# Kernel tuning notes

Hardware: AMD Instinct MI355X
Metric: run time of the kernel (lower is better)

Reference implementation:

```python
import jax, jax.numpy as jnp
import numpy as np

D_MODEL = 1024
EXPAND = 2
D_INNER = EXPAND * D_MODEL  # 2048
D_STATE = 16
D_CONV = 4
DT_RANK = D_INNER  # non-int dt_rank resolves to d_inner
BATCH, SEQ = 2, 1024
EPS = 1e-5


def setup_inputs() -> dict:
    key = jax.random.key(0)
    ks = jax.random.split(key, 9)
    s = 0.02
    return {
        "x": jax.random.normal(ks[0], (BATCH, SEQ, D_MODEL), jnp.float32),
        "rms_w": jnp.ones((D_MODEL,), jnp.float32),
        "W_in": jax.random.normal(ks[1], (D_MODEL, 2 * D_INNER), jnp.float32) * s,
        "conv_w": jax.random.normal(ks[2], (D_INNER, 1, D_CONV), jnp.float32) * 0.2,
        "conv_b": jax.random.normal(ks[3], (D_INNER,), jnp.float32) * 0.02,
        "W_x": jax.random.normal(ks[4], (D_INNER, DT_RANK + 2 * D_STATE), jnp.float32) * s,
        "W_dt": jax.random.normal(ks[5], (DT_RANK, D_INNER), jnp.float32) * s,
        "A_log": jax.random.normal(ks[6], (D_INNER, D_STATE), jnp.float32),
        "W_out": jax.random.normal(ks[7], (D_INNER, D_MODEL), jnp.float32) * s,
    }


def _rmsnorm(x, w):
    var = jnp.mean(jnp.square(x), axis=-1, keepdims=True)
    return x * jax.lax.rsqrt(var + EPS) * w


def _forward(x, rms_w, W_in, conv_w, conv_b, W_x, W_dt, A_log, W_out):
    B, L, _ = x.shape
    residual = x
    xn = _rmsnorm(x, rms_w)
    xr = xn @ W_in                                  # [B,L,2*d_inner]
    xs, res = jnp.split(xr, 2, axis=-1)
    # causal depthwise conv1d: torch pads d_conv-1 both sides then slices [:L]
    xc = jnp.transpose(xs, (0, 2, 1))               # [B,d_inner,L]
    xc = jnp.pad(xc, ((0, 0), (0, 0), (D_CONV - 1, 0)))
    xc = jax.lax.conv_general_dilated(
        xc, conv_w, window_strides=(1,), padding='VALID',
        dimension_numbers=('NCH', 'OIH', 'NCH'), feature_group_count=D_INNER)
    xc = xc + conv_b[None, :, None]
    xs = jax.nn.silu(jnp.transpose(xc, (0, 2, 1)))  # [B,L,d_inner]
    x_ssm = xs @ W_x                                # [B,L,d_inner+2*d_state]
    dt, Bm, Cm = jnp.split(x_ssm, [D_INNER, D_INNER + D_STATE], axis=-1)
    dt = jax.nn.softplus(dt @ W_dt)                 # [B,L,d_inner]
    A = -jnp.exp(A_log)                             # [d_inner,d_state]
    A_disc = jnp.exp(A[None, None] * dt[..., None])            # [B,L,d_inner,N]
    Bx = dt[..., None] * Bm[:, :, None, :] * xs[..., None]     # [B,L,d_inner,N]

    def step(h, inp):
        Ad_t, Bx_t, C_t = inp                       # [B,d_inner,N],[B,d_inner,N],[B,N]
        h = Ad_t * h + Bx_t
        y = jnp.einsum('bdn,bn->bd', h, C_t)
        return h, y

    h0 = jnp.zeros((B, D_INNER, D_STATE), xs.dtype)
    _, ys = jax.lax.scan(
        step, h0,
        (jnp.transpose(A_disc, (1, 0, 2, 3)),
         jnp.transpose(Bx, (1, 0, 2, 3)),
         jnp.transpose(Cm, (1, 0, 2))))
    y = jnp.transpose(ys, (1, 0, 2))                # [B,L,d_inner]
    y = y * jax.nn.silu(res)
    out = y @ W_out
    return residual + out


def reference(x, rms_w, W_in, conv_w, conv_b, W_x, W_dt, A_log, W_out):
    return _forward(x, rms_w, W_in, conv_w, conv_b, W_x, W_dt, A_log, W_out)
```

## Files before the change

### kernel.cpp

```cpp
#include <hip/hip_runtime.h>
#include <math.h>

#define B_SZ   2
#define LSEQ   1024
#define DMODEL 1024
#define DINNER 2048
#define DSTATE 16
#define NTOK   (B_SZ * LSEQ)
#define NSSM   (DINNER + 2 * DSTATE)
#define CL     16
#define NCH    (LSEQ / CL)
#define NC     (B_SZ * DINNER)

typedef unsigned short ushort;
typedef __attribute__((ext_vector_type(8))) ushort ushort8;
typedef __attribute__((ext_vector_type(8))) __bf16 bf16x8;
typedef __attribute__((ext_vector_type(4))) float floatx4;

__device__ __forceinline__ float softplus_f(float x) {
  return (x > 20.f) ? x : __logf(1.f + __expf(x));
}
__device__ __forceinline__ float silu_f(float x) {
  return x / (1.f + __expf(-x));
}
__device__ __forceinline__ float bf2f(ushort u) {
  return __uint_as_float(((unsigned)u) << 16);
}
__device__ __forceinline__ ushort f2bf(float f) {
  unsigned u = __float_as_uint(f);
  return (ushort)((u + 0x7FFFu + ((u >> 16) & 1u)) >> 16);
}

__global__ __launch_bounds__(256) void rmsnorm_kernel(
    const float* __restrict__ x, const float* __restrict__ w,
    ushort* __restrict__ xn) {
  int row = blockIdx.x;
  const float* xrow = x + (size_t)row * DMODEL;
  float v[4];
  float ss = 0.f;
#pragma unroll
  for (int i = 0; i < 4; i++) {
    v[i] = xrow[threadIdx.x + 256 * i];
    ss += v[i] * v[i];
  }
  __shared__ float wsum[4];
  int lane = threadIdx.x & 63, wid = threadIdx.x >> 6;
#pragma unroll
  for (int off = 1; off < 64; off <<= 1) ss += __shfl_xor(ss, off);
  if (lane == 0) wsum[wid] = ss;
  __syncthreads();
  float tot = wsum[0] + wsum[1] + wsum[2] + wsum[3];
  float scale = rsqrtf(tot / (float)DMODEL + 1e-5f);
#pragma unroll
  for (int i = 0; i < 4; i++) {
    int j = threadIdx.x + 256 * i;
    xn[(size_t)row * DMODEL + j] = f2bf(v[i] * scale * w[j]);
  }
}

__global__ __launch_bounds__(256) void transpose_all(
    const float* __restrict__ Win, ushort* __restrict__ WinT,
    const float* __restrict__ Wx, ushort* __restrict__ WxT,
    const float* __restrict__ Wdt, ushort* __restrict__ WdtT,
    const float* __restrict__ Wout, ushort* __restrict__ WoutT) {
  int blk = blockIdx.x;
  const float* W; ushort* Wt; int K, N, nb, idx;
  if (blk < 1024)      { W = Win;  Wt = WinT;  K = DMODEL; N = 4096;  nb = 64; idx = blk; }
  else if (blk < 2080) { W = Wx;   Wt = WxT;   K = DINNER; N = NSSM;  nb = 33; idx = blk - 1024; }
  else if (blk < 3104) { W = Wdt;  Wt = WdtT;  K = DINNER; N = DINNER;nb = 32; idx = blk - 2080; }
  else                 { W = Wout; Wt = WoutT; K = DINNER; N = DMODEL;nb = 16; idx = blk - 3104; }
  int n0 = (idx % nb) * 64, k0 = (idx / nb) * 64;
  __shared__ float tile[64][65];
  int c = threadIdx.x & 63, rb = (threadIdx.x >> 6) << 4;
#pragma unroll
  for (int i = 0; i < 16; i++) {
    int k = k0 + rb + i;
    if (k < K && n0 + c < N) tile[rb + i][c] = W[(size_t)k * N + n0 + c];
  }
  __syncthreads();
#pragma unroll
  for (int i = 0; i < 16; i++) {
    int n = n0 + rb + i;
    if (n < N && k0 + c < K)
      Wt[(size_t)n * K + k0 + c] = f2bf(tile[c][rb + i]);
  }
}

__global__ __launch_bounds__(256, 3) void gemm_mfma(
    const ushort* __restrict__ A, int lda,
    const ushort* __restrict__ Bt, int ldb,
    int N, int K, int mode,
    void* __restrict__ C0, void* __restrict__ C1,
    const float* __restrict__ addend) {
  __shared__ ushort As[2 * 2 * 128 * 32];
  __shared__ ushort Bs[2 * 2 * 64 * 32];
  const int bm = blockIdx.y * 128, bn = blockIdx.x * 64;
  const int tid = threadIdx.x;
  const int wave = tid >> 6, lane = tid & 63;
  const int wm = (wave & 1) << 6, wn = (wave >> 1) << 5;
  const int lrow = lane & 15, quad = lane >> 4;
  const size_t koff = (size_t)blockIdx.z * K;

  const int sr = tid >> 2;
  const int q  = tid & 3;
  const int swr = (sr ^ (sr >> 2)) & 3;
  const int pq = (q ^ swr) << 3;
  const int brow = min(bn + sr, N - 1);
  const ushort* ga0 = A + (size_t)(bm + sr) * lda + koff + (q << 3);
  const ushort* ga1 = A + (size_t)(bm + sr + 64) * lda + koff + (q << 3);
  const ushort* gb0 = Bt + (size_t)brow * ldb + koff + (q << 3);

  floatx4 acc[4][2];
#pragma unroll
  for (int i = 0; i < 4; i++)
#pragma unroll
    for (int j = 0; j < 2; j++) acc[i][j] = (floatx4){0.f, 0.f, 0.f, 0.f};

  const int swf = ((lrow ^ (lrow >> 2)) & 3);
  const int fq = ((quad ^ swf) << 3);

  const int nk = K >> 6;
  ushort8 ra[2][2], rbv[2];
#pragma unroll
  for (int p = 0; p < 2; p++) {
    ra[p][0] = *(const ushort8*)(ga0 + p * 32);
    ra[p][1] = *(const ushort8*)(ga1 + p * 32);
    rbv[p]   = *(const ushort8*)(gb0 + p * 32);
  }
  for (int kt = 0; kt < nk; kt++) {
    const int boA = (kt & 1) << 13;
    const int boB = (kt & 1) << 12;
#pragma unroll
    for (int p = 0; p < 2; p++) {
      *(ushort8*)&As[boA + (p << 12) + sr * 32 + pq] = ra[p][0];
      *(ushort8*)&As[boA + (p << 12) + (sr + 64) * 32 + pq] = ra[p][1];
      *(ushort8*)&Bs[boB + (p << 11) + sr * 32 + pq] = rbv[p];
    }
    __syncthreads();
    if (kt + 1 < nk) {
      const int ko = (kt + 1) << 6;
#pragma unroll
      for (int p = 0; p < 2; p++) {
        ra[p][0] = *(const ushort8*)(ga0 + ko + p * 32);
        ra[p][1] = *(const ushort8*)(ga1 + ko + p * 32);
        rbv[p]   = *(const ushort8*)(gb0 + ko + p * 32);
      }
    }
#pragma unroll
    for (int p = 0; p < 2; p++) {
      bf16x8 af[4], bfr[2];
#pragma unroll
      for (int i = 0; i < 4; i++)
        af[i] = __builtin_bit_cast(bf16x8,
            *(const ushort8*)&As[boA + (p << 12) + (wm + i * 16 + lrow) * 32 + fq]);
#pragma unroll
      for (int j = 0; j < 2; j++)
        bfr[j] = __builtin_bit_cast(bf16x8,
            *(const ushort8*)&Bs[boB + (p << 11) + (wn + j * 16 + lrow) * 32 + fq]);
#pragma unroll
      for (int i = 0; i < 4; i++)
#pragma unroll
        for (int j = 0; j < 2; j++)
          acc[i][j] = __builtin_amdgcn_mfma_f32_16x16x32_bf16(
              af[i], bfr[j], acc[i][j], 0, 0, 0);
    }
  }
  const int m0 = bm + wm, n0 = bn + wn, rq = quad << 2;
  float* P = (float*)C0 + (size_t)blockIdx.z * NTOK * N;
#pragma unroll
  for (int i = 0; i < 4; i++) {
#pragma unroll
    for (int j = 0; j < 2; j++) {
#pragma unroll
      for (int r = 0; r < 4; r++) {
        int m = m0 + i * 16 + rq + r;
        int n = n0 + j * 16 + lrow;
        if (n >= N) continue;
        float v = acc[i][j][r];
        if (mode == 0) {
          P[(size_t)m * N + n] = v;
        } else if (mode == 1) {
          if (n < DINNER)
            ((ushort*)C0)[(size_t)m * DINNER + n] = f2bf(v);
          else
            ((ushort*)C1)[(size_t)m * DINNER + n - DINNER] = f2bf(silu_f(v));
        } else if (mode == 2) {
          ((ushort*)C0)[(size_t)m * NSSM + n] = f2bf(v);
          if (n >= DINNER)
            ((float*)C1)[(size_t)m * 32 + n - DINNER] = v;
        } else {
          ((float*)C0)[(size_t)m * DINNER + n] = softplus_f(v);
        }
      }
    }
  }
}

__global__ __launch_bounds__(256) void reduce_wout(
    const float* __restrict__ P, const float* __restrict__ x,
    float* __restrict__ out) {
  int gid = blockIdx.x * 256 + threadIdx.x;
  const float4 a = ((const float4*)P)[gid];
  const float4 b = ((const float4*)P)[gid + (NTOK * DMODEL / 4)];
  const float4 r = ((const float4*)x)[gid];
  ((float4*)out)[gid] = make_float4(a.x + b.x + r.x, a.y + b.y + r.y,
                                    a.z + b.z + r.z, a.w + b.w + r.w);
}

__global__ __launch_bounds__(256) void conv_silu_kernel(
    const ushort* __restrict__ xsraw, const float* __restrict__ cw,
    const float* __restrict__ cb, ushort* __restrict__ xs) {
  int gid = blockIdx.x * 256 + threadIdx.x;
  int c = gid & (DINNER - 1);
  int t = gid >> 11;
  int l = t & (LSEQ - 1);
  float w0 = cw[c * 4 + 0], w1 = cw[c * 4 + 1], w2 = cw[c * 4 + 2], w3 = cw[c * 4 + 3];
  const ushort* col = xsraw + (size_t)t * DINNER + c;
  float acc = cb[c] + w3 * bf2f(col[0]);
  if (l >= 1) acc += w2 * bf2f(col[-DINNER]);
  if (l >= 2) acc += w1 * bf2f(col[-2 * DINNER]);
  if (l >= 3) acc += w0 * bf2f(col[-3 * DINNER]);
  xs[gid] = f2bf(silu_f(acc));
}

__global__ __launch_bounds__(256) void scan_chunk1(
    const float* __restrict__ dt, const ushort* __restrict__ xs,
    const float* __restrict__ bc, const float* __restrict__ A_log,
    float* __restrict__ Bc, float* __restrict__ S) {
  int blk = blockIdx.x;
  int b = blk >> 9;
  int rem = blk & 511;
  int ch = rem >> 3;
  int dblk = rem & 7;
  int d = dblk * 256 + threadIdx.x;
  int c = b * DINNER + d;
  float a[DSTATE];
#pragma unroll
  for (int i = 0; i < 4; i++) {
    float4 v = *(const float4*)(A_log + (size_t)d * DSTATE + 4 * i);
    a[4 * i + 0] = -__expf(v.x);
    a[4 * i + 1] = -__expf(v.y);
    a[4 * i + 2] = -__expf(v.z);
    a[4 * i + 3] = -__expf(v.w);
  }
  float h[DSTATE] = {};
  float Ssum = 0.f;
  size_t t = (size_t)b * LSEQ + (size_t)ch * CL;
#pragma unroll 2
  for (int l = 0; l < CL; l++, t++) {
    float dtv = dt[t * DINNER + d];
    float dx = dtv * bf2f(xs[t * DINNER + d]);
    const float4* Bp = (const float4*)(bc + t * 32);
    float4 b0 = Bp[0], b1 = Bp[1], b2 = Bp[2], b3 = Bp[3];
    float bb[DSTATE] = {b0.x, b0.y, b0.z, b0.w, b1.x, b1.y, b1.z, b1.w,
                        b2.x, b2.y, b2.z, b2.w, b3.x, b3.y, b3.z, b3.w};
#pragma unroll
    for (int n = 0; n < DSTATE; n++)
      h[n] = __expf(a[n] * dtv) * h[n] + dx * bb[n];
    Ssum += dtv;
  }
  float4* outp = (float4*)(Bc + ((size_t)c * NCH + ch) * DSTATE);
  outp[0] = make_float4(h[0], h[1], h[2], h[3]);
  outp[1] = make_float4(h[4], h[5], h[6], h[7]);
  outp[2] = make_float4(h[8], h[9], h[10], h[11]);
  outp[3] = make_float4(h[12], h[13], h[14], h[15]);
  S[c * NCH + ch] = Ssum;
}

__global__ __launch_bounds__(256) void scan_combine(
    const float* __restrict__ A_log, const float* __restrict__ S,
    float* BcHin) {
  int gid = blockIdx.x * 256 + threadIdx.x;
  int c = gid >> 4, n = gid & 15;
  int d = c & (DINNER - 1);
  float a = -__expf(A_log[d * DSTATE + n]);
  float h = 0.f;
  size_t base = (size_t)c * (NCH * DSTATE) + n;
  for (int ch = 0; ch < NCH; ch++) {
    float bcv = BcHin[base + (size_t)ch * DSTATE];
    float decay = __expf(a * S[c * NCH + ch]);
    BcHin[base + (size_t)ch * DSTATE] = h;
    h = decay * h + bcv;
  }
}

__global__ __launch_bounds__(256) void scan_chunk2(
    const float* __restrict__ dt, const ushort* __restrict__ xs,
    const float* __restrict__ bc, const ushort* __restrict__ gate,
    const float* __restrict__ A_log, const float* __restrict__ hin,
    ushort* __restrict__ y) {
  int blk = blockIdx.x;
  int b = blk >> 9;
  int rem = blk & 511;
  int ch = rem >> 3;
  int dblk = rem & 7;
  int d = dblk * 256 + threadIdx.x;
  int c = b * DINNER + d;
  float a[DSTATE];
#pragma unroll
  for (int i = 0; i < 4; i++) {
    float4 v = *(const float4*)(A_log + (size_t)d * DSTATE + 4 * i);
    a[4 * i + 0] = -__expf(v.x);
    a[4 * i + 1] = -__expf(v.y);
    a[4 * i + 2] = -__expf(v.z);
    a[4 * i + 3] = -__expf(v.w);
  }
  float h[DSTATE];
  const float4* hi = (const float4*)(hin + ((size_t)c * NCH + ch) * DSTATE);
#pragma unroll
  for (int i = 0; i < 4; i++) {
    float4 v = hi[i];
    h[4 * i + 0] = v.x; h[4 * i + 1] = v.y; h[4 * i + 2] = v.z; h[4 * i + 3] = v.w;
  }
  size_t t = (size_t)b * LSEQ + (size_t)ch * CL;
#pragma unroll 2
  for (int l = 0; l < CL; l++, t++) {
    float dtv = dt[t * DINNER + d];
    float dx = dtv * bf2f(xs[t * DINNER + d]);
    const float4* Bp = (const float4*)(bc + t * 32);
    const float4* Cp = (const float4*)(bc + t * 32 + 16);
    float4 b0 = Bp[0], b1 = Bp[1], b2 = Bp[2], b3 = Bp[3];
    float4 c0 = Cp[0], c1 = Cp[1], c2 = Cp[2], c3 = Cp[3];
    float bb[DSTATE] = {b0.x, b0.y, b0.z, b0.w, b1.x, b1.y, b1.z, b1.w,
                        b2.x, b2.y, b2.z, b2.w, b3.x, b3.y, b3.z, b3.w};
    float cc[DSTATE] = {c0.x, c0.y, c0.z, c0.w, c1.x, c1.y, c1.z, c1.w,
                        c2.x, c2.y, c2.z, c2.w, c3.x, c3.y, c3.z, c3.w};
    float ysum = 0.f;
#pragma unroll
    for (int n = 0; n < DSTATE; n++) {
      h[n] = __expf(a[n] * dtv) * h[n] + dx * bb[n];
      ysum = fmaf(h[n], cc[n], ysum);
    }
    y[t * DINNER + d] = f2bf(ysum * bf2f(gate[t * DINNER + d]));
  }
}

extern "C" void kernel_launch(void* const* d_in, const int* in_sizes, int n_in,
                              void* d_out, int out_size, void* d_ws, size_t ws_size,
                              hipStream_t stream) {
  const float* x      = (const float*)d_in[0];
  const float* rms_w  = (const float*)d_in[1];
  const float* W_in   = (const float*)d_in[2];
  const float* conv_w = (const float*)d_in[3];
  const float* conv_b = (const float*)d_in[4];
  const float* W_x    = (const float*)d_in[5];
  const float* W_dt   = (const float*)d_in[6];
  const float* A_log  = (const float*)d_in[7];
  const float* W_out  = (const float*)d_in[8];
  float* out = (float*)d_out;

  char* w = (char*)d_ws;
  ushort* xnb   = (ushort*)(w + 0);
  ushort* xsraw = (ushort*)(w + 4194304);
  ushort* gate  = (ushort*)(w + 12582912);
  ushort* xsb   = (ushort*)(w + 20971520);
  ushort* ssmb  = (ushort*)(w + 29360128);
  float*  dtb   = (float*)(w + 37879808);
  ushort* yb    = (ushort*)(w + 54657024);
  ushort* WinT  = (ushort*)(w + 63045632);
  ushort* WxT   = (ushort*)(w + 71434240);
  ushort* WdtT  = (ushort*)(w + 79953920);
  ushort* WoutT = (ushort*)(w + 88342528);
  float* bc = (float*)(w + 0);
  float* Bc = (float*)(w + 63045632);
  float* S  = (float*)(w + 79953920);
  float* P  = (float*)(w + 4194304);

  transpose_all<<<3616, 256, 0, stream>>>(W_in, WinT, W_x, WxT, W_dt, WdtT, W_out, WoutT);

  rmsnorm_kernel<<<NTOK, 256, 0, stream>>>(x, rms_w, xnb);
  gemm_mfma<<<dim3(64, 16), 256, 0, stream>>>(
      xnb, DMODEL, WinT, DMODEL, 4096, DMODEL, 1, xsraw, gate, nullptr);
  conv_silu_kernel<<<(NTOK * DINNER) / 256, 256, 0, stream>>>(xsraw, conv_w, conv_b, xsb);
  gemm_mfma<<<dim3(33, 16), 256, 0, stream>>>(
      xsb, DINNER, WxT, DINNER, NSSM, DINNER, 2, ssmb, bc, nullptr);
  gemm_mfma<<<dim3(32, 16), 256, 0, stream>>>(
      ssmb, NSSM, WdtT, DINNER, DINNER, DINNER, 3, dtb, nullptr, nullptr);
  scan_chunk1<<<B_SZ * NCH * 8, 256, 0, stream>>>(dtb, xsb, bc, A_log, Bc, S);
  scan_combine<<<(NC * DSTATE) / 256, 256, 0, stream>>>(A_log, S, Bc);
  scan_chunk2<<<B_SZ * NCH * 8, 256, 0, stream>>>(dtb, xsb, bc, gate, A_log, Bc, yb);
  gemm_mfma<<<dim3(16, 16, 2), 256, 0, stream>>>(
      yb, DINNER, WoutT, DINNER, DMODEL, DINNER / 2, 0, P, nullptr, nullptr);
  reduce_wout<<<(NTOK * DMODEL / 4) / 256, 256, 0, stream>>>(P, x, out);
}
```

Before: 327.2 us.

## Load GEMM B fragments directly from global into registers; fuse rmsnorm into prep kernel

The GEMM kernel stops staging the B (weight) tile in shared memory. Each wave now loads its own B fragments straight from global memory into registers and double-buffers them across k-steps, which cuts LDS traffic and frees shared memory. The cost is redundant global loads, since the two waves sharing a column block both fetch the same B data, and loads that are less coalesced. Separately, rmsnorm is folded into the weight-transpose launch as extra blocks, saving one kernel launch.

New measurement: 387.0 us. 18.3% more time.

```diff
diff --git a/kernel.cpp b/kernel.cpp
--- a/kernel.cpp
+++ b/kernel.cpp
@@ -31,39 +31,39 @@
   return (ushort)((u + 0x7FFFu + ((u >> 16) & 1u)) >> 16);
 }
 
-__global__ __launch_bounds__(256) void rmsnorm_kernel(
-    const float* __restrict__ x, const float* __restrict__ w,
-    ushort* __restrict__ xn) {
-  int row = blockIdx.x;
-  const float* xrow = x + (size_t)row * DMODEL;
-  float v[4];
-  float ss = 0.f;
-#pragma unroll
-  for (int i = 0; i < 4; i++) {
-    v[i] = xrow[threadIdx.x + 256 * i];
-    ss += v[i] * v[i];
-  }
-  __shared__ float wsum[4];
-  int lane = threadIdx.x & 63, wid = threadIdx.x >> 6;
-#pragma unroll
-  for (int off = 1; off < 64; off <<= 1) ss += __shfl_xor(ss, off);
-  if (lane == 0) wsum[wid] = ss;
-  __syncthreads();
-  float tot = wsum[0] + wsum[1] + wsum[2] + wsum[3];
-  float scale = rsqrtf(tot / (float)DMODEL + 1e-5f);
-#pragma unroll
-  for (int i = 0; i < 4; i++) {
-    int j = threadIdx.x + 256 * i;
-    xn[(size_t)row * DMODEL + j] = f2bf(v[i] * scale * w[j]);
-  }
-}
-
-__global__ __launch_bounds__(256) void transpose_all(
+__global__ __launch_bounds__(256) void prep_all(
     const float* __restrict__ Win, ushort* __restrict__ WinT,
     const float* __restrict__ Wx, ushort* __restrict__ WxT,
     const float* __restrict__ Wdt, ushort* __restrict__ WdtT,
-    const float* __restrict__ Wout, ushort* __restrict__ WoutT) {
+    const float* __restrict__ Wout, ushort* __restrict__ WoutT,
+    const float* __restrict__ x, const float* __restrict__ rw,
+    ushort* __restrict__ xn) {
   int blk = blockIdx.x;
+  if (blk >= 3616) {
+    int row = blk - 3616;
+    const float* xrow = x + (size_t)row * DMODEL;
+    float v[4];
+    float ss = 0.f;
+#pragma unroll
+    for (int i = 0; i < 4; i++) {
+      v[i] = xrow[threadIdx.x + 256 * i];
+      ss += v[i] * v[i];
+    }
+    __shared__ float wsum[4];
+    int lane = threadIdx.x & 63, wid = threadIdx.x >> 6;
+#pragma unroll
+    for (int off = 1; off < 64; off <<= 1) ss += __shfl_xor(ss, off);
+    if (lane == 0) wsum[wid] = ss;
+    __syncthreads();
+    float tot = wsum[0] + wsum[1] + wsum[2] + wsum[3];
+    float scale = rsqrtf(tot / (float)DMODEL + 1e-5f);
+#pragma unroll
+    for (int i = 0; i < 4; i++) {
+      int j = threadIdx.x + 256 * i;
+      xn[(size_t)row * DMODEL + j] = f2bf(v[i] * scale * rw[j]);
+    }
+    return;
+  }
   const float* W; ushort* Wt; int K, N, nb, idx;
   if (blk < 1024)      { W = Win;  Wt = WinT;  K = DMODEL; N = 4096;  nb = 64; idx = blk; }
   else if (blk < 2080) { W = Wx;   Wt = WxT;   K = DINNER; N = NSSM;  nb = 33; idx = blk - 1024; }
@@ -93,7 +93,6 @@
     void* __restrict__ C0, void* __restrict__ C1,
     const float* __restrict__ addend) {
   __shared__ ushort As[2 * 2 * 128 * 32];
-  __shared__ ushort Bs[2 * 2 * 64 * 32];
   const int bm = blockIdx.y * 128, bn = blockIdx.x * 64;
   const int tid = threadIdx.x;
   const int wave = tid >> 6, lane = tid & 63;
@@ -105,10 +104,15 @@
   const int q  = tid & 3;
   const int swr = (sr ^ (sr >> 2)) & 3;
   const int pq = (q ^ swr) << 3;
-  const int brow = min(bn + sr, N - 1);
   const ushort* ga0 = A + (size_t)(bm + sr) * lda + koff + (q << 3);
   const ushort* ga1 = A + (size_t)(bm + sr + 64) * lda + koff + (q << 3);
-  const ushort* gb0 = Bt + (size_t)brow * ldb + koff + (q << 3);
+
+  const ushort* gb[2];
+#pragma unroll
+  for (int j = 0; j < 2; j++) {
+    int brow = min(bn + wn + j * 16 + lrow, N - 1);
+    gb[j] = Bt + (size_t)brow * ldb + koff + (quad << 3);
+  }
 
   floatx4 acc[4][2];
 #pragma unroll
@@ -120,49 +124,54 @@
   const int fq = ((quad ^ swf) << 3);
 
   const int nk = K >> 6;
-  ushort8 ra[2][2], rbv[2];
+  ushort8 ra[2][2];
+  ushort8 bcur[2][2];
 #pragma unroll
   for (int p = 0; p < 2; p++) {
     ra[p][0] = *(const ushort8*)(ga0 + p * 32);
     ra[p][1] = *(const ushort8*)(ga1 + p * 32);
-    rbv[p]   = *(const ushort8*)(gb0 + p * 32);
+#pragma unroll
+    for (int j = 0; j < 2; j++) bcur[p][j] = *(const ushort8*)(gb[j] + p * 32);
   }
   for (int kt = 0; kt < nk; kt++) {
-    const int boA = (kt & 1) << 13;
-    const int boB = (kt & 1) << 12;
+    const int bo = (kt & 1) << 13;
 #pragma unroll
     for (int p = 0; p < 2; p++) {
-      *(ushort8*)&As[boA + (p << 12) + sr * 32 + pq] = ra[p][0];
-      *(ushort8*)&As[boA + (p << 12) + (sr + 64) * 32 + pq] = ra[p][1];
-      *(ushort8*)&Bs[boB + (p << 11) + sr * 32 + pq] = rbv[p];
+      *(ushort8*)&As[bo + (p << 12) + sr * 32 + pq] = ra[p][0];
+      *(ushort8*)&As[bo + (p << 12) + (sr + 64) * 32 + pq] = ra[p][1];
     }
     __syncthreads();
+    ushort8 bnxt[2][2];
     if (kt + 1 < nk) {
       const int ko = (kt + 1) << 6;
 #pragma unroll
       for (int p = 0; p < 2; p++) {
         ra[p][0] = *(const ushort8*)(ga0 + ko + p * 32);
         ra[p][1] = *(const ushort8*)(ga1 + ko + p * 32);
-        rbv[p]   = *(const ushort8*)(gb0 + ko + p * 32);
+#pragma unroll
+        for (int j = 0; j < 2; j++)
+          bnxt[p][j] = *(const ushort8*)(gb[j] + ko + p * 32);
       }
     }
 #pragma unroll
     for (int p = 0; p < 2; p++) {
-      bf16x8 af[4], bfr[2];
+      bf16x8 af[4];
 #pragma unroll
       for (int i = 0; i < 4; i++)
         af[i] = __builtin_bit_cast(bf16x8,
-            *(const ushort8*)&As[boA + (p << 12) + (wm + i * 16 + lrow) * 32 + fq]);
-#pragma unroll
-      for (int j = 0; j < 2; j++)
-        bfr[j] = __builtin_bit_cast(bf16x8,
-            *(const ushort8*)&Bs[boB + (p << 11) + (wn + j * 16 + lrow) * 32 + fq]);
+            *(const ushort8*)&As[bo + (p << 12) + (wm + i * 16 + lrow) * 32 + fq]);
 #pragma unroll
       for (int i = 0; i < 4; i++)
 #pragma unroll
         for (int j = 0; j < 2; j++)
           acc[i][j] = __builtin_amdgcn_mfma_f32_16x16x32_bf16(
-              af[i], bfr[j], acc[i][j], 0, 0, 0);
+              af[i], __builtin_bit_cast(bf16x8, bcur[p][j]), acc[i][j], 0, 0, 0);
+    }
+    if (kt + 1 < nk) {
+#pragma unroll
+      for (int p = 0; p < 2; p++)
+#pragma unroll
+        for (int j = 0; j < 2; j++) bcur[p][j] = bnxt[p][j];
     }
   }
   const int m0 = bm + wm, n0 = bn + wn, rq = quad << 2;
@@ -366,9 +375,9 @@
   float* S  = (float*)(w + 79953920);
   float* P  = (float*)(w + 4194304);
 
-  transpose_all<<<3616, 256, 0, stream>>>(W_in, WinT, W_x, WxT, W_dt, WdtT, W_out, WoutT);
-
-  rmsnorm_kernel<<<NTOK, 256, 0, stream>>>(x, rms_w, xnb);
+  prep_all<<<3616 + NTOK, 256, 0, stream>>>(
+      W_in, WinT, W_x, WxT, W_dt, WdtT, W_out, WoutT, x, rms_w, xnb);
+
   gemm_mfma<<<dim3(64, 16), 256, 0, stream>>>(
       xnb, DMODEL, WinT, DMODEL, 4096, DMODEL, 1, xsraw, gate, nullptr);
   conv_silu_kernel<<<(NTOK * DINNER) / 256, 256, 0, stream>>>(xsraw, conv_w, conv_b, xsb);
```
